# Optimization experiments

Measured on AMD Instinct MI355X. Metric: run time of the kernel, lower is better.

Reference implementation:

```python
import jax, jax.numpy as jnp
import numpy as np

GENE_NUM = 3000
N_NODES = 50000
N_EDGES = 1000000
DIM = 128


def setup_inputs() -> dict:
    key = jax.random.key(0)
    ks = jax.random.split(key, 8)
    h = jax.random.normal(ks[0], (N_NODES, DIM), dtype=jnp.float32)
    alpha = jax.random.normal(ks[1], (GENE_NUM + 2,), dtype=jnp.float32)
    edge_weight = jax.random.uniform(ks[2], (N_EDGES,), dtype=jnp.float32)
    # Xavier-uniform Linear weight, zero bias
    gain = float(np.sqrt(2.0))  # calculate_gain('relu')
    bound = gain * np.sqrt(6.0 / (DIM + DIM))
    W = jax.random.uniform(ks[3], (DIM, DIM), minval=-bound, maxval=bound, dtype=jnp.float32)
    b = jnp.zeros((DIM,), dtype=jnp.float32)
    # node ids: genes 0..GENE_NUM-1 have id = gene index (>=0); cells have id = -1 (<0)
    node_id = jnp.concatenate([
        jnp.arange(GENE_NUM, dtype=jnp.int64),
        -jnp.ones((N_NODES - GENE_NUM,), dtype=jnp.int64),
    ])
    edge_src = jax.random.randint(ks[4], (N_EDGES,), 0, N_NODES, dtype=jnp.int64)
    edge_dst = jax.random.randint(ks[5], (N_EDGES,), 0, N_NODES, dtype=jnp.int64)
    return {"h": h, "alpha": alpha, "edge_weight": edge_weight, "W": W, "b": b,
            "node_id": node_id, "edge_src": edge_src, "edge_dst": edge_dst}


def reference(h, alpha, edge_weight, W, b, node_id, edge_src, edge_dst):
    gene_num = alpha.shape[0] - 2
    src_id = node_id[edge_src]  # [E]
    dst_id = node_id[edge_dst]  # [E]
    # default: cell self-loop alpha -> index gene_num + 1
    idx = jnp.full(edge_src.shape, gene_num + 1, dtype=jnp.int32)
    idx = jnp.where((src_id >= 0) & (dst_id < 0), src_id.astype(jnp.int32), idx)   # gene->cell: beta[src]
    idx = jnp.where((dst_id >= 0) & (src_id < 0), dst_id.astype(jnp.int32), idx)   # cell->gene: beta[dst]
    idx = jnp.where((dst_id >= 0) & (src_id >= 0), gene_num, idx)                  # gene self-loop alpha
    # gather -> per-edge message [E, D]
    coeff = alpha[idx] * edge_weight                     # [E]
    msg = h[edge_src] * coeff[:, None]                   # [E, D]
    # scatter-mean over destination nodes
    n = h.shape[0]
    summ = jax.ops.segment_sum(msg, edge_dst, num_segments=n)           # [N, D]
    cnt = jax.ops.segment_sum(jnp.ones_like(edge_weight), edge_dst, num_segments=n)
    neigh = summ / jnp.maximum(cnt, 1.0)[:, None]
    # MLP: dropout(eval, identity) -> Linear -> ReLU -> norm(identity)
    z = jax.nn.relu(neigh @ W.T + b)
    return z
```

## Files before the change

kernel.cpp:

```cpp
#include <hip/hip_runtime.h>

#define D 128
#define PSHIFT 6
#define PSIZE 64
#define EDGES_PER_BLK 4096
#define CAP 2048
#define PSTRIDE 2240
#define MAXPART 1024
#define NCHUNK 4

typedef __attribute__((ext_vector_type(8))) short bf16x8;
typedef __attribute__((ext_vector_type(4))) float f32x4;

__device__ __forceinline__ unsigned short f2bf(float f) {
  unsigned int u = __float_as_uint(f);
  u = (u + 0x7fffu + ((u >> 16) & 1)) >> 16;
  return (unsigned short)u;
}

__global__ __launch_bounds__(512) void cvt_hist_kernel(
    const float* __restrict__ h, unsigned short* __restrict__ h16, int total4,
    const int* __restrict__ edst, int* __restrict__ g_hist, int E,
    int cvtBlocks, int N) {
  if ((int)blockIdx.x < cvtBlocks) {
    int i = blockIdx.x * 512 + threadIdx.x;
    if (i >= total4) return;
    float4 v = ((const float4*)h)[i];
    ushort4 o;
    o.x = f2bf(v.x); o.y = f2bf(v.y); o.z = f2bf(v.z); o.w = f2bf(v.w);
    int f = i * 4;
    int n = f >> 7;
    int d = f & 127;
    int c = d >> 5;
    int wi = d & 31;
    ((ushort4*)h16)[(size_t)c * N * 8 + n * 8 + (wi >> 2)] = o;
    return;
  }
  __shared__ int cnt[MAXPART];
  int t = threadIdx.x;
  cnt[t] = 0; cnt[t + 512] = 0;
  __syncthreads();
  int eb = (blockIdx.x - cvtBlocks) * EDGES_PER_BLK;
#pragma unroll
  for (int q = 0; q < 8; ++q) {
    int e = eb + q * 512 + t;
    if (e < E) atomicAdd(&cnt[edst[e] >> PSHIFT], 1);
  }
  __syncthreads();
  int c = cnt[t];
  if (c > 0) atomicAdd(&g_hist[t], c);
  c = cnt[t + 512];
  if (c > 0) atomicAdd(&g_hist[t + 512], c);
}

__global__ __launch_bounds__(512) void part_scan_kernel(
    const int* __restrict__ g_hist, int* __restrict__ part_off,
    int* __restrict__ g_cursor, int E, int npart) {
  __shared__ int ts[512];
  int t = threadIdx.x;
  int i0 = 2 * t, i1 = 2 * t + 1;
  int v0 = (i0 < npart) ? g_hist[i0] : 0;
  int v1 = (i1 < npart) ? g_hist[i1] : 0;
  ts[t] = v0 + v1;
  __syncthreads();
  for (int off = 1; off < 512; off <<= 1) {
    int x = (t >= off) ? ts[t - off] : 0;
    __syncthreads();
    ts[t] += x;
    __syncthreads();
  }
  int excl = ts[t] - (v0 + v1);
  if (i0 < npart) { part_off[i0] = excl; g_cursor[i0] = excl; }
  if (i1 < npart) { part_off[i1] = excl + v0; g_cursor[i1] = excl + v0; }
  if (t == 0) part_off[npart] = E;
}

__global__ __launch_bounds__(512) void bin_scatter_kernel(
    const float* __restrict__ alpha, const float* __restrict__ ew,
    const int* __restrict__ node_id, const int* __restrict__ esrc,
    const int* __restrict__ edst, int* __restrict__ g_cursor,
    unsigned int* __restrict__ recs4, unsigned char* __restrict__ dl8,
    int E, int gene_num) {
  __shared__ unsigned int lrec[EDGES_PER_BLK];
  __shared__ unsigned short lbin[EDGES_PER_BLK];
  __shared__ unsigned char ldl[EDGES_PER_BLK];
  __shared__ int cnt[MAXPART], offl[MAXPART], gbase[MAXPART];
  __shared__ int ts[512];

  int t = threadIdx.x;
  cnt[t] = 0; cnt[t + 512] = 0;
  __syncthreads();

  int eb = blockIdx.x * EDGES_PER_BLK;
  unsigned int rx[8]; int rb[8]; int rk[8]; int rdl[8];
#pragma unroll
  for (int q = 0; q < 8; ++q) {
    int e = eb + q * 512 + t;
    rk[q] = -1;
    if (e < E) {
      int src = esrc[e];
      int dst = edst[e];
      int sid = node_id[src];
      int did = node_id[dst];
      int idx;
      if (sid >= 0) idx = (did >= 0) ? gene_num : sid;
      else          idx = (did >= 0) ? did : (gene_num + 1);
      float coeff = alpha[idx] * ew[e];
      rx[q] = (unsigned int)src | ((unsigned int)f2bf(coeff) << 16);
      rdl[q] = dst & (PSIZE - 1);
      int b = dst >> PSHIFT;
      rb[q] = b;
      rk[q] = atomicAdd(&cnt[b], 1);
    }
  }
  __syncthreads();

  int c0 = cnt[2 * t], c1 = cnt[2 * t + 1];
  ts[t] = c0 + c1;
  __syncthreads();
  for (int off = 1; off < 512; off <<= 1) {
    int x = (t >= off) ? ts[t - off] : 0;
    __syncthreads();
    ts[t] += x;
    __syncthreads();
  }
  int exclp = ts[t] - (c0 + c1);
  offl[2 * t] = exclp;
  offl[2 * t + 1] = exclp + c0;
  __syncthreads();

#pragma unroll
  for (int q = 0; q < 8; ++q) {
    if (rk[q] >= 0) {
      int ls = offl[rb[q]] + rk[q];
      lrec[ls] = rx[q];
      lbin[ls] = (unsigned short)rb[q];
      ldl[ls] = (unsigned char)rdl[q];
    }
  }
  __syncthreads();

  {
    int c = cnt[t];
    if (c > 0) gbase[t] = atomicAdd(&g_cursor[t], c);
    c = cnt[t + 512];
    if (c > 0) gbase[t + 512] = atomicAdd(&g_cursor[t + 512], c);
  }
  __syncthreads();

  int tot = E - eb;
  if (tot > EDGES_PER_BLK) tot = EDGES_PER_BLK;
  for (int s = t; s < tot; s += 512) {
    int b = lbin[s];
    int pos = gbase[b] + (s - offl[b]);
    recs4[pos] = lrec[s];
    dl8[pos] = ldl[s];
  }
}

__global__ __launch_bounds__(512) void sort_kernel(
    const unsigned int* __restrict__ recs4, const unsigned char* __restrict__ dl8,
    const int* __restrict__ part_off, unsigned int* __restrict__ recs4p,
    int* __restrict__ cnt_g, int* __restrict__ pad_g, int* __restrict__ rk_g) {
  __shared__ unsigned int lrec[PSTRIDE];
  __shared__ int cnt[PSIZE], padl[PSIZE];

  int t = threadIdx.x;
  int p = blockIdx.x;
  if (t < PSIZE) cnt[t] = 0;
  for (int s = t; s < PSTRIDE; s += 512) lrec[s] = 0u;
  __syncthreads();

  int start = part_off[p];
  int R = part_off[p + 1] - start;
  if (R > CAP) R = CAP;

  unsigned int rq[4]; int dlq[4]; int rkq[4];
#pragma unroll
  for (int q = 0; q < 4; ++q) {
    int s = q * 512 + t;
    rkq[q] = -1;
    if (s < R) {
      rq[q] = recs4[start + s];
      int dl = dl8[start + s];
      dlq[q] = dl;
      rkq[q] = atomicAdd(&cnt[dl], 1);
    }
  }
  __syncthreads();

  if (t < PSIZE) padl[t] = (cnt[t] + 3) & ~3;
  __syncthreads();
  for (int off = 1; off < PSIZE; off <<= 1) {
    int x = 0;
    if (t < PSIZE && t >= off) x = padl[t - off];
    __syncthreads();
    if (t < PSIZE) padl[t] += x;
    __syncthreads();
  }
  if (t < PSIZE) padl[t] -= (cnt[t] + 3) & ~3;
  __syncthreads();

#pragma unroll
  for (int q = 0; q < 4; ++q)
    if (rkq[q] >= 0) lrec[padl[dlq[q]] + rkq[q]] = rq[q];
  __syncthreads();

  int padTot = padl[PSIZE - 1] + ((cnt[PSIZE - 1] + 3) & ~3);
  for (int s = t; s < padTot; s += 512)
    recs4p[(size_t)p * PSTRIDE + s] = lrec[s];
  if (t < PSIZE) {
    cnt_g[p * PSIZE + t] = cnt[t];
    pad_g[p * PSIZE + t] = padl[t];
    int my = cnt[t];
    int r = 0;
    for (int j = 0; j < PSIZE; ++j) {
      int cj = cnt[j];
      r += (cj > my) || (cj == my && j < t);
    }
    rk_g[p * PSIZE + r] = t;
  }
}

__global__ __launch_bounds__(512) void part_acc_kernel(
    const unsigned short* __restrict__ h16, const unsigned int* __restrict__ recs4p,
    const int* __restrict__ cnt_g, const int* __restrict__ pad_g,
    const int* __restrict__ rk_g, float* __restrict__ neigh, int N) {
  __shared__ unsigned int lrec[PSTRIDE];

  int t = threadIdx.x;
  int p = blockIdx.x >> 2;
  int chunk = blockIdx.x & 3;

  int padTot = pad_g[p * PSIZE + PSIZE - 1] +
               ((cnt_g[p * PSIZE + PSIZE - 1] + 3) & ~3);
  for (int s = t; s < padTot; s += 512)
    lrec[s] = recs4p[(size_t)p * PSTRIDE + s];
  __syncthreads();

  int w = t >> 6;
  int l = t & 63;
  int esub = l >> 4;
  int dpair = l & 15;
  const unsigned int* hpc =
      ((const unsigned int*)h16) + (size_t)chunk * N * 16 + dpair;

#pragma unroll
  for (int h2 = 0; h2 < 2; ++h2) {
    int Q = (h2 == 0) ? w : (15 - w);
    int myDl = rk_g[p * PSIZE + Q * 4 + esub];
    int myCnt = cnt_g[p * PSIZE + myDl];
    int myOff = pad_g[p * PSIZE + myDl];
    int myPad = (myCnt + 3) & ~3;
    float ax = 0.f, ay = 0.f;
    int k = 0;
    for (; k + 8 <= myPad; k += 8) {
      unsigned int v[8]; float c[8];
#pragma unroll
      for (int q = 0; q < 8; ++q) {
        unsigned int r = lrec[myOff + k + q];
        c[q] = __uint_as_float(r & 0xffff0000u);
        v[q] = hpc[(size_t)(r & 0xffffu) * 16];
      }
#pragma unroll
      for (int q = 0; q < 8; ++q) {
        ax += c[q] * __uint_as_float(v[q] << 16);
        ay += c[q] * __uint_as_float(v[q] & 0xffff0000u);
      }
    }
    if (k < myPad) {
      unsigned int v[4]; float c[4];
#pragma unroll
      for (int q = 0; q < 4; ++q) {
        unsigned int r = lrec[myOff + k + q];
        c[q] = __uint_as_float(r & 0xffff0000u);
        v[q] = hpc[(size_t)(r & 0xffffu) * 16];
      }
#pragma unroll
      for (int q = 0; q < 4; ++q) {
        ax += c[q] * __uint_as_float(v[q] << 16);
        ay += c[q] * __uint_as_float(v[q] & 0xffff0000u);
      }
    }
    int dst = p * PSIZE + myDl;
    if (dst < N) {
      float inv = 1.0f / (float)(myCnt > 0 ? myCnt : 1);
      ((float2*)neigh)[(size_t)dst * 64 + chunk * 16 + dpair] =
          make_float2(ax * inv, ay * inv);
    }
  }
}

__global__ __launch_bounds__(256) void mlp_mfma_kernel(
    const float* __restrict__ W, const float* __restrict__ bias,
    float* __restrict__ io, int N) {
  __shared__ __align__(16) unsigned short Wl[128 * 128];

  int t = threadIdx.x;
#pragma unroll
  for (int i = 0; i < 8; ++i) {
    int chunk = t + 256 * i;
    int row = chunk >> 4;
    int cb = chunk & 15;
    const float* gp = W + (size_t)row * 128 + cb * 8;
    float4 a = *(const float4*)gp;
    float4 b = *(const float4*)(gp + 4);
    bf16x8 v;
    v[0] = (short)f2bf(a.x); v[1] = (short)f2bf(a.y);
    v[2] = (short)f2bf(a.z); v[3] = (short)f2bf(a.w);
    v[4] = (short)f2bf(b.x); v[5] = (short)f2bf(b.y);
    v[6] = (short)f2bf(b.z); v[7] = (short)f2bf(b.w);
    *(bf16x8*)((char*)Wl + row * 256 + ((cb ^ (row & 7)) << 4)) = v;
  }
  __syncthreads();

  int l = t & 63;
  int w = t >> 6;
  int kg = l >> 4;
  int m_base = blockIdx.x * 64 + w * 16;
  int arow = m_base + (l & 15);
  if (arow >= N) arow = N - 1;

  bf16x8 af[4];
  const float* ap = io + (size_t)arow * 128 + kg * 8;
#pragma unroll
  for (int kk = 0; kk < 4; ++kk) {
    float4 a = *(const float4*)(ap + kk * 32);
    float4 b = *(const float4*)(ap + kk * 32 + 4);
    bf16x8 v;
    v[0] = (short)f2bf(a.x); v[1] = (short)f2bf(a.y);
    v[2] = (short)f2bf(a.z); v[3] = (short)f2bf(a.w);
    v[4] = (short)f2bf(b.x); v[5] = (short)f2bf(b.y);
    v[6] = (short)f2bf(b.z); v[7] = (short)f2bf(b.w);
    af[kk] = v;
  }

#pragma unroll
  for (int c = 0; c < 8; ++c) {
    f32x4 acc = {0.f, 0.f, 0.f, 0.f};
    int row_w = c * 16 + (l & 15);
    int rs = row_w & 7;
#pragma unroll
    for (int kk = 0; kk < 4; ++kk) {
      int cb = kk * 4 + kg;
      bf16x8 bf = *(bf16x8*)((char*)Wl + row_w * 256 + ((cb ^ rs) << 4));
      acc = __builtin_amdgcn_mfma_f32_16x16x32_bf16(af[kk], bf, acc, 0, 0, 0);
    }
    int j = c * 16 + (l & 15);
    float bj = bias[j];
#pragma unroll
    for (int r = 0; r < 4; ++r) {
      int m = m_base + kg * 4 + r;
      if (m < N) io[(size_t)m * 128 + j] = fmaxf(acc[r] + bj, 0.0f);
    }
  }
}

extern "C" void kernel_launch(void* const* d_in, const int* in_sizes, int n_in,
                              void* d_out, int out_size, void* d_ws, size_t ws_size,
                              hipStream_t stream) {
  const float* h     = (const float*)d_in[0];
  const float* alpha = (const float*)d_in[1];
  const float* ew    = (const float*)d_in[2];
  const float* W     = (const float*)d_in[3];
  const float* bias  = (const float*)d_in[4];
  const int* node_id = (const int*)d_in[5];
  const int* esrc    = (const int*)d_in[6];
  const int* edst    = (const int*)d_in[7];
  float* out = (float*)d_out;

  int E = in_sizes[2];
  int N = in_sizes[5];
  int gene_num = in_sizes[1] - 2;
  int npart = (N + PSIZE - 1) / PSIZE;
  int eblocks = (E + EDGES_PER_BLK - 1) / EDGES_PER_BLK;
  int total4 = N * D / 4;
  int cvtBlocks = (total4 + 511) / 512;

  int* g_hist   = (int*)d_ws;
  int* part_off = g_hist + MAXPART;
  int* g_cursor = part_off + MAXPART + 1;
  int* cnt_g    = g_cursor + MAXPART;
  int* pad_g    = cnt_g + MAXPART * PSIZE;
  int* rk_g     = pad_g + MAXPART * PSIZE;
  size_t h16_off = ((size_t)(3 * MAXPART + 1 + 3 * MAXPART * PSIZE) * sizeof(int)
                    + 15) & ~(size_t)15;
  unsigned short* h16 = (unsigned short*)((char*)d_ws + h16_off);
  size_t r4_off = (h16_off + (size_t)N * D * sizeof(unsigned short) + 15) & ~(size_t)15;
  unsigned int* recs4 = (unsigned int*)((char*)d_ws + r4_off);
  size_t dl_off = (r4_off + (size_t)(E + 8) * 4 + 15) & ~(size_t)15;
  unsigned char* dl8 = (unsigned char*)((char*)d_ws + dl_off);
  size_t r4p_off = (dl_off + (size_t)(E + 8) + 15) & ~(size_t)15;
  unsigned int* recs4p = (unsigned int*)((char*)d_ws + r4p_off);
  size_t need = r4p_off + (size_t)npart * PSTRIDE * 4;
  if (ws_size < need) return;

  hipMemsetAsync(g_hist, 0, MAXPART * sizeof(int), stream);

  cvt_hist_kernel<<<cvtBlocks + eblocks, 512, 0, stream>>>(
      h, h16, total4, edst, g_hist, E, cvtBlocks, N);
  part_scan_kernel<<<1, 512, 0, stream>>>(g_hist, part_off, g_cursor, E, npart);
  bin_scatter_kernel<<<eblocks, 512, 0, stream>>>(alpha, ew, node_id, esrc,
                                                  edst, g_cursor, recs4, dl8,
                                                  E, gene_num);
  sort_kernel<<<npart, 512, 0, stream>>>(recs4, dl8, part_off, recs4p,
                                         cnt_g, pad_g, rk_g);
  part_acc_kernel<<<npart * NCHUNK, 512, 0, stream>>>(h16, recs4p, cnt_g,
                                                      pad_g, rk_g, out, N);
  {
    int blocks = (N + 63) / 64;
    mlp_mfma_kernel<<<blocks, 256, 0, stream>>>(W, bias, out, N);
  }
}
```

Baseline: 109.1 us.

## Widen per-lane gathers in partition accumulate kernel and halve block size

The accumulate kernel now gives each lane 4 bf16 features through 8-byte loads, with 8 lanes per destination row instead of 16. Edge records are read from LDS as uint4 vectors. The block shrinks to 256 threads, so each block still covers 64 destinations in two passes. The aim is fewer, wider gather instructions and fewer LDS reads, at the cost of less parallelism per destination and possibly less latency hiding.

```diff
diff --git a/kernel.cpp b/kernel.cpp
--- a/kernel.cpp
+++ b/kernel.cpp
@@ -222,11 +222,11 @@
   }
 }
 
-__global__ __launch_bounds__(512) void part_acc_kernel(
+__global__ __launch_bounds__(256) void part_acc_kernel(
     const unsigned short* __restrict__ h16, const unsigned int* __restrict__ recs4p,
     const int* __restrict__ cnt_g, const int* __restrict__ pad_g,
     const int* __restrict__ rk_g, float* __restrict__ neigh, int N) {
-  __shared__ unsigned int lrec[PSTRIDE];
+  __shared__ __align__(16) unsigned int lrec[PSTRIDE];
 
   int t = threadIdx.x;
   int p = blockIdx.x >> 2;
@@ -234,59 +234,110 @@
 
   int padTot = pad_g[p * PSIZE + PSIZE - 1] +
                ((cnt_g[p * PSIZE + PSIZE - 1] + 3) & ~3);
-  for (int s = t; s < padTot; s += 512)
+  for (int s = t; s < padTot; s += 256)
     lrec[s] = recs4p[(size_t)p * PSTRIDE + s];
   __syncthreads();
 
   int w = t >> 6;
   int l = t & 63;
-  int esub = l >> 4;
-  int dpair = l & 15;
+  int g = l >> 3;
+  int lane8 = l & 7;
   const unsigned int* hpc =
-      ((const unsigned int*)h16) + (size_t)chunk * N * 16 + dpair;
-
-#pragma unroll
-  for (int h2 = 0; h2 < 2; ++h2) {
-    int Q = (h2 == 0) ? w : (15 - w);
-    int myDl = rk_g[p * PSIZE + Q * 4 + esub];
+      ((const unsigned int*)h16) + (size_t)chunk * N * 16 + lane8 * 2;
+
+#pragma unroll
+  for (int pass = 0; pass < 2; ++pass) {
+    int rank = (pass == 0) ? (w * 8 + g) : (63 - (w * 8 + g));
+    int myDl = rk_g[p * PSIZE + rank];
     int myCnt = cnt_g[p * PSIZE + myDl];
     int myOff = pad_g[p * PSIZE + myDl];
     int myPad = (myCnt + 3) & ~3;
-    float ax = 0.f, ay = 0.f;
+    float a0 = 0.f, a1 = 0.f, a2 = 0.f, a3 = 0.f;
     int k = 0;
     for (; k + 8 <= myPad; k += 8) {
-      unsigned int v[8]; float c[8];
-#pragma unroll
-      for (int q = 0; q < 8; ++q) {
-        unsigned int r = lrec[myOff + k + q];
-        c[q] = __uint_as_float(r & 0xffff0000u);
-        v[q] = hpc[(size_t)(r & 0xffffu) * 16];
-      }
-#pragma unroll
-      for (int q = 0; q < 8; ++q) {
-        ax += c[q] * __uint_as_float(v[q] << 16);
-        ay += c[q] * __uint_as_float(v[q] & 0xffff0000u);
-      }
+      uint4 ra = *(const uint4*)&lrec[myOff + k];
+      uint4 rb = *(const uint4*)&lrec[myOff + k + 4];
+      uint2 v0 = *(const uint2*)(hpc + (size_t)(ra.x & 0xffffu) * 16);
+      uint2 v1 = *(const uint2*)(hpc + (size_t)(ra.y & 0xffffu) * 16);
+      uint2 v2 = *(const uint2*)(hpc + (size_t)(ra.z & 0xffffu) * 16);
+      uint2 v3 = *(const uint2*)(hpc + (size_t)(ra.w & 0xffffu) * 16);
+      uint2 v4 = *(const uint2*)(hpc + (size_t)(rb.x & 0xffffu) * 16);
+      uint2 v5 = *(const uint2*)(hpc + (size_t)(rb.y & 0xffffu) * 16);
+      uint2 v6 = *(const uint2*)(hpc + (size_t)(rb.z & 0xffffu) * 16);
+      uint2 v7 = *(const uint2*)(hpc + (size_t)(rb.w & 0xffffu) * 16);
+      float c0 = __uint_as_float(ra.x & 0xffff0000u);
+      float c1 = __uint_as_float(ra.y & 0xffff0000u);
+      float c2 = __uint_as_float(ra.z & 0xffff0000u);
+      float c3 = __uint_as_float(ra.w & 0xffff0000u);
+      float c4 = __uint_as_float(rb.x & 0xffff0000u);
+      float c5 = __uint_as_float(rb.y & 0xffff0000u);
+      float c6 = __uint_as_float(rb.z & 0xffff0000u);
+      float c7 = __uint_as_float(rb.w & 0xffff0000u);
+      a0 += c0 * __uint_as_float(v0.x << 16);
+      a1 += c0 * __uint_as_float(v0.x & 0xffff0000u);
+      a2 += c0 * __uint_as_float(v0.y << 16);
+      a3 += c0 * __uint_as_float(v0.y & 0xffff0000u);
+      a0 += c1 * __uint_as_float(v1.x << 16);
+      a1 += c1 * __uint_as_float(v1.x & 0xffff0000u);
+      a2 += c1 * __uint_as_float(v1.y << 16);
+      a3 += c1 * __uint_as_float(v1.y & 0xffff0000u);
+      a0 += c2 * __uint_as_float(v2.x << 16);
+      a1 += c2 * __uint_as_float(v2.x & 0xffff0000u);
+      a2 += c2 * __uint_as_float(v2.y << 16);
+      a3 += c2 * __uint_as_float(v2.y & 0xffff0000u);
+      a0 += c3 * __uint_as_float(v3.x << 16);
+      a1 += c3 * __uint_as_float(v3.x & 0xffff0000u);
+      a2 += c3 * __uint_as_float(v3.y << 16);
+      a3 += c3 * __uint_as_float(v3.y & 0xffff0000u);
+      a0 += c4 * __uint_as_float(v4.x << 16);
+      a1 += c4 * __uint_as_float(v4.x & 0xffff0000u);
+      a2 += c4 * __uint_as_float(v4.y << 16);
+      a3 += c4 * __uint_as_float(v4.y & 0xffff0000u);
+      a0 += c5 * __uint_as_float(v5.x << 16);
+      a1 += c5 * __uint_as_float(v5.x & 0xffff0000u);
+      a2 += c5 * __uint_as_float(v5.y << 16);
+      a3 += c5 * __uint_as_float(v5.y & 0xffff0000u);
+      a0 += c6 * __uint_as_float(v6.x << 16);
+      a1 += c6 * __uint_as_float(v6.x & 0xffff0000u);
+      a2 += c6 * __uint_as_float(v6.y << 16);
+      a3 += c6 * __uint_as_float(v6.y & 0xffff0000u);
+      a0 += c7 * __uint_as_float(v7.x << 16);
+      a1 += c7 * __uint_as_float(v7.x & 0xffff0000u);
+      a2 += c7 * __uint_as_float(v7.y << 16);
+      a3 += c7 * __uint_as_float(v7.y & 0xffff0000u);
     }
     if (k < myPad) {
-      unsigned int v[4]; float c[4];
-#pragma unroll
-      for (int q = 0; q < 4; ++q) {
-        unsigned int r = lrec[myOff + k + q];
-        c[q] = __uint_as_float(r & 0xffff0000u);
-        v[q] = hpc[(size_t)(r & 0xffffu) * 16];
-      }
-#pragma unroll
-      for (int q = 0; q < 4; ++q) {
-        ax += c[q] * __uint_as_float(v[q] << 16);
-        ay += c[q] * __uint_as_float(v[q] & 0xffff0000u);
-      }
+      uint4 ra = *(const uint4*)&lrec[myOff + k];
+      uint2 v0 = *(const uint2*)(hpc + (size_t)(ra.x & 0xffffu) * 16);
+      uint2 v1 = *(const uint2*)(hpc + (size_t)(ra.y & 0xffffu) * 16);
+      uint2 v2 = *(const uint2*)(hpc + (size_t)(ra.z & 0xffffu) * 16);
+      uint2 v3 = *(const uint2*)(hpc + (size_t)(ra.w & 0xffffu) * 16);
+      float c0 = __uint_as_float(ra.x & 0xffff0000u);
+      float c1 = __uint_as_float(ra.y & 0xffff0000u);
+      float c2 = __uint_as_float(ra.z & 0xffff0000u);
+      float c3 = __uint_as_float(ra.w & 0xffff0000u);
+      a0 += c0 * __uint_as_float(v0.x << 16);
+      a1 += c0 * __uint_as_float(v0.x & 0xffff0000u);
+      a2 += c0 * __uint_as_float(v0.y << 16);
+      a3 += c0 * __uint_as_float(v0.y & 0xffff0000u);
+      a0 += c1 * __uint_as_float(v1.x << 16);
+      a1 += c1 * __uint_as_float(v1.x & 0xffff0000u);
+      a2 += c1 * __uint_as_float(v1.y << 16);
+      a3 += c1 * __uint_as_float(v1.y & 0xffff0000u);
+      a0 += c2 * __uint_as_float(v2.x << 16);
+      a1 += c2 * __uint_as_float(v2.x & 0xffff0000u);
+      a2 += c2 * __uint_as_float(v2.y << 16);
+      a3 += c2 * __uint_as_float(v2.y & 0xffff0000u);
+      a0 += c3 * __uint_as_float(v3.x << 16);
+      a1 += c3 * __uint_as_float(v3.x & 0xffff0000u);
+      a2 += c3 * __uint_as_float(v3.y << 16);
+      a3 += c3 * __uint_as_float(v3.y & 0xffff0000u);
     }
     int dst = p * PSIZE + myDl;
     if (dst < N) {
       float inv = 1.0f / (float)(myCnt > 0 ? myCnt : 1);
-      ((float2*)neigh)[(size_t)dst * 64 + chunk * 16 + dpair] =
-          make_float2(ax * inv, ay * inv);
+      float4 o = make_float4(a0 * inv, a1 * inv, a2 * inv, a3 * inv);
+      ((float4*)neigh)[(size_t)dst * 32 + chunk * 8 + lane8] = o;
     }
   }
 }
@@ -405,7 +456,7 @@
                                                   E, gene_num);
   sort_kernel<<<npart, 512, 0, stream>>>(recs4, dl8, part_off, recs4p,
                                          cnt_g, pad_g, rk_g);
-  part_acc_kernel<<<npart * NCHUNK, 512, 0, stream>>>(h16, recs4p, cnt_g,
+  part_acc_kernel<<<npart * NCHUNK, 256, 0, stream>>>(h16, recs4p, cnt_g,
                                                       pad_g, rk_g, out, N);
   {
     int blocks = (N + 63) / 64;
```

After: 106.4 us. 1.03x faster.

## Widen gather to 16-byte loads with 4 lanes per destination in accumulate kernel

Applied to the files above, without the earlier changes.

The partition accumulate kernel now assigns 4 lanes per destination node, each gathering a uint4 (8 bf16 values) instead of 16 lanes each loading one 32-bit word. Records are read from LDS as uint4 vectors, accumulation uses packed float2 FMAs, and the output is written as float4. The block shrinks to 256 threads, so each thread handles one destination instead of two. The aim is fewer, wider gather and LDS instructions per edge. In exchange it uses more registers per thread and gives less lane-level parallelism per row.

```diff
diff --git a/kernel.cpp b/kernel.cpp
--- a/kernel.cpp
+++ b/kernel.cpp
@@ -11,6 +11,7 @@
 
 typedef __attribute__((ext_vector_type(8))) short bf16x8;
 typedef __attribute__((ext_vector_type(4))) float f32x4;
+typedef __attribute__((ext_vector_type(2))) float f32x2;
 
 __device__ __forceinline__ unsigned short f2bf(float f) {
   unsigned int u = __float_as_uint(f);
@@ -222,11 +223,11 @@
   }
 }
 
-__global__ __launch_bounds__(512) void part_acc_kernel(
+__global__ __launch_bounds__(256) void part_acc_kernel(
     const unsigned short* __restrict__ h16, const unsigned int* __restrict__ recs4p,
     const int* __restrict__ cnt_g, const int* __restrict__ pad_g,
     const int* __restrict__ rk_g, float* __restrict__ neigh, int N) {
-  __shared__ unsigned int lrec[PSTRIDE];
+  __shared__ __align__(16) unsigned int lrec[PSTRIDE];
 
   int t = threadIdx.x;
   int p = blockIdx.x >> 2;
@@ -234,60 +235,75 @@
 
   int padTot = pad_g[p * PSIZE + PSIZE - 1] +
                ((cnt_g[p * PSIZE + PSIZE - 1] + 3) & ~3);
-  for (int s = t; s < padTot; s += 512)
+  for (int s = t; s < padTot; s += 256)
     lrec[s] = recs4p[(size_t)p * PSTRIDE + s];
   __syncthreads();
 
   int w = t >> 6;
   int l = t & 63;
-  int esub = l >> 4;
-  int dpair = l & 15;
-  const unsigned int* hpc =
-      ((const unsigned int*)h16) + (size_t)chunk * N * 16 + dpair;
-
-#pragma unroll
-  for (int h2 = 0; h2 < 2; ++h2) {
-    int Q = (h2 == 0) ? w : (15 - w);
-    int myDl = rk_g[p * PSIZE + Q * 4 + esub];
-    int myCnt = cnt_g[p * PSIZE + myDl];
-    int myOff = pad_g[p * PSIZE + myDl];
-    int myPad = (myCnt + 3) & ~3;
-    float ax = 0.f, ay = 0.f;
-    int k = 0;
-    for (; k + 8 <= myPad; k += 8) {
-      unsigned int v[8]; float c[8];
-#pragma unroll
-      for (int q = 0; q < 8; ++q) {
-        unsigned int r = lrec[myOff + k + q];
-        c[q] = __uint_as_float(r & 0xffff0000u);
-        v[q] = hpc[(size_t)(r & 0xffffu) * 16];
-      }
-#pragma unroll
-      for (int q = 0; q < 8; ++q) {
-        ax += c[q] * __uint_as_float(v[q] << 16);
-        ay += c[q] * __uint_as_float(v[q] & 0xffff0000u);
-      }
-    }
-    if (k < myPad) {
-      unsigned int v[4]; float c[4];
-#pragma unroll
-      for (int q = 0; q < 4; ++q) {
-        unsigned int r = lrec[myOff + k + q];
-        c[q] = __uint_as_float(r & 0xffff0000u);
-        v[q] = hpc[(size_t)(r & 0xffffu) * 16];
-      }
-#pragma unroll
-      for (int q = 0; q < 4; ++q) {
-        ax += c[q] * __uint_as_float(v[q] << 16);
-        ay += c[q] * __uint_as_float(v[q] & 0xffff0000u);
-      }
-    }
-    int dst = p * PSIZE + myDl;
-    if (dst < N) {
-      float inv = 1.0f / (float)(myCnt > 0 ? myCnt : 1);
-      ((float2*)neigh)[(size_t)dst * 64 + chunk * 16 + dpair] =
-          make_float2(ax * inv, ay * inv);
-    }
+  int g = l >> 2;
+  int l4 = l & 3;
+  int rank = (g < 8) ? (w * 8 + g) : (63 - (w * 8 + (g - 8)));
+  int myDl = rk_g[p * PSIZE + rank];
+  int myCnt = cnt_g[p * PSIZE + myDl];
+  int myOff = pad_g[p * PSIZE + myDl];
+  int myPad = (myCnt + 3) & ~3;
+
+  const uint4* hpc4 =
+      (const uint4*)(((const unsigned int*)h16) + (size_t)chunk * N * 16);
+
+  f32x2 a0 = {0.f, 0.f}, a1 = {0.f, 0.f}, a2 = {0.f, 0.f}, a3 = {0.f, 0.f};
+
+#define ACC_REC(RW, VV)                                                      \
+  {                                                                          \
+    float cf = __uint_as_float((RW) & 0xffff0000u);                          \
+    f32x2 c2 = {cf, cf};                                                     \
+    f32x2 p0 = {__uint_as_float((VV).x << 16),                               \
+                __uint_as_float((VV).x & 0xffff0000u)};                      \
+    f32x2 p1 = {__uint_as_float((VV).y << 16),                               \
+                __uint_as_float((VV).y & 0xffff0000u)};                      \
+    f32x2 p2 = {__uint_as_float((VV).z << 16),                               \
+                __uint_as_float((VV).z & 0xffff0000u)};                      \
+    f32x2 p3 = {__uint_as_float((VV).w << 16),                               \
+                __uint_as_float((VV).w & 0xffff0000u)};                      \
+    a0 = c2 * p0 + a0;                                                       \
+    a1 = c2 * p1 + a1;                                                       \
+    a2 = c2 * p2 + a2;                                                       \
+    a3 = c2 * p3 + a3;                                                       \
+  }
+
+  int k = 0;
+  for (; k + 8 <= myPad; k += 8) {
+    uint4 ra = *(const uint4*)&lrec[myOff + k];
+    uint4 rb = *(const uint4*)&lrec[myOff + k + 4];
+    uint4 v0 = hpc4[(size_t)(ra.x & 0xffffu) * 4 + l4];
+    uint4 v1 = hpc4[(size_t)(ra.y & 0xffffu) * 4 + l4];
+    uint4 v2 = hpc4[(size_t)(ra.z & 0xffffu) * 4 + l4];
+    uint4 v3 = hpc4[(size_t)(ra.w & 0xffffu) * 4 + l4];
+    uint4 v4 = hpc4[(size_t)(rb.x & 0xffffu) * 4 + l4];
+    uint4 v5 = hpc4[(size_t)(rb.y & 0xffffu) * 4 + l4];
+    uint4 v6 = hpc4[(size_t)(rb.z & 0xffffu) * 4 + l4];
+    uint4 v7 = hpc4[(size_t)(rb.w & 0xffffu) * 4 + l4];
+    ACC_REC(ra.x, v0); ACC_REC(ra.y, v1); ACC_REC(ra.z, v2); ACC_REC(ra.w, v3);
+    ACC_REC(rb.x, v4); ACC_REC(rb.y, v5); ACC_REC(rb.z, v6); ACC_REC(rb.w, v7);
+  }
+  if (k < myPad) {
+    uint4 ra = *(const uint4*)&lrec[myOff + k];
+    uint4 v0 = hpc4[(size_t)(ra.x & 0xffffu) * 4 + l4];
+    uint4 v1 = hpc4[(size_t)(ra.y & 0xffffu) * 4 + l4];
+    uint4 v2 = hpc4[(size_t)(ra.z & 0xffffu) * 4 + l4];
+    uint4 v3 = hpc4[(size_t)(ra.w & 0xffffu) * 4 + l4];
+    ACC_REC(ra.x, v0); ACC_REC(ra.y, v1); ACC_REC(ra.z, v2); ACC_REC(ra.w, v3);
+  }
+#undef ACC_REC
+
+  int dst = p * PSIZE + myDl;
+  if (dst < N) {
+    float inv = 1.0f / (float)(myCnt > 0 ? myCnt : 1);
+    float4 o0 = make_float4(a0.x * inv, a0.y * inv, a1.x * inv, a1.y * inv);
+    float4 o1 = make_float4(a2.x * inv, a2.y * inv, a3.x * inv, a3.y * inv);
+    ((float4*)neigh)[(size_t)dst * 32 + chunk * 8 + l4 * 2] = o0;
+    ((float4*)neigh)[(size_t)dst * 32 + chunk * 8 + l4 * 2 + 1] = o1;
   }
 }
 
@@ -405,7 +421,7 @@
                                                   E, gene_num);
   sort_kernel<<<npart, 512, 0, stream>>>(recs4, dl8, part_off, recs4p,
                                          cnt_g, pad_g, rk_g);
-  part_acc_kernel<<<npart * NCHUNK, 512, 0, stream>>>(h16, recs4p, cnt_g,
+  part_acc_kernel<<<npart * NCHUNK, 256, 0, stream>>>(h16, recs4p, cnt_g,
                                                       pad_g, rk_g, out, N);
   {
     int blocks = (N + 63) / 64;
```

Measured after the change: 107.1 us. Within noise of the previous version (-1.9%).
